# Optimization experiments

Measured on AMD Instinct MI355X. Metric: run time of the kernel, lower is better.

The kernel has to match this reference:

```python
import jax, jax.numpy as jnp
import numpy as np

H = 8          # num_heads
D = 64         # head_dim
HID = 512      # hidden_size
W = 128        # window_size
NEG = -1e9

def setup_inputs() -> dict:
    key = jax.random.key(0)
    ks = jax.random.split(key, 12)
    B, S = 2, 2048
    def lin(i):
        w = jax.random.normal(ks[i], (HID, HID), dtype=jnp.float32) * (1.0 / np.sqrt(HID))
        b = jax.random.normal(ks[i + 1], (HID,), dtype=jnp.float32) * 0.01
        return w, b
    Wq, bq = lin(0)
    Wk, bk = lin(2)
    Wv, bv = lin(4)
    Wo, bo = lin(6)
    return {
        "value": jax.random.normal(ks[8], (B, S, HID), dtype=jnp.float32),
        "key": jax.random.normal(ks[9], (B, S, HID), dtype=jnp.float32),
        "query": jax.random.normal(ks[10], (B, S, HID), dtype=jnp.float32),
        "Wq": Wq, "bq": bq, "Wk": Wk, "bk": bk,
        "Wv": Wv, "bv": bv, "Wo": Wo, "bo": bo,
    }

def reference(value, key, query, Wq, bq, Wk, bk, Wv, bv, Wo, bo):
    B, S, _ = query.shape
    def heads(x, Wt, b):
        # torch Linear: x @ W.T + b ; then [B,S,H,D] -> [B,H,S,D]
        return (x @ Wt.T + b).reshape(B, S, H, D).transpose(0, 2, 1, 3)
    Q = heads(query, Wq, bq)
    K = heads(key, Wk, bk)
    V = heads(value, Wv, bv)
    scores = jnp.einsum('bhqd,bhkd->bhqk', Q, K) / jnp.sqrt(jnp.float32(D))
    idx = jnp.arange(S)
    local = jnp.abs(idx[:, None] - idx[None, :]) <= W  # [S,S] band mask
    scores = jnp.where(local[None, None], scores, NEG)
    weights = jax.nn.softmax(scores, axis=-1)
    out = jnp.einsum('bhqk,bhkd->bhqd', weights, V)
    out = out.transpose(0, 2, 1, 3).reshape(B, S, HID)
    return out @ Wo.T + bo
```

## Files before the change

kernel.cpp:

```cpp
#include <hip/hip_runtime.h>
#include <stdint.h>

#define B_   2
#define S_   2048
#define H_   8
#define D_   64
#define HID_ 512
#define W_   128
#define M_   (B_ * S_)
#define E_   (M_ * HID_)
#define WSZ_ (HID_ * HID_)
#define PPAD_ 72
#define M0_  12.0f

typedef unsigned short u16;
typedef __attribute__((ext_vector_type(8))) __bf16 bf16x8;
typedef __attribute__((ext_vector_type(4))) float  floatx4;

__device__ __forceinline__ u16 f2b(float f) {
    union { __bf16 b; u16 u; } x;
    x.b = (__bf16)f;
    return x.u;
}

__device__ __forceinline__ void gll16(const u16* g, u16* l) {
    __builtin_amdgcn_global_load_lds(
        (const __attribute__((address_space(1))) unsigned int*)g,
        (__attribute__((address_space(3))) unsigned int*)l, 16, 0, 0);
}

__device__ __forceinline__ void cvt8_store(float4 a, float4 b, u16* dst) {
    bf16x8 v;
    v[0] = (__bf16)a.x; v[1] = (__bf16)a.y; v[2] = (__bf16)a.z; v[3] = (__bf16)a.w;
    v[4] = (__bf16)b.x; v[5] = (__bf16)b.y; v[6] = (__bf16)b.z; v[7] = (__bf16)b.w;
    *(bf16x8*)dst = v;
}

__global__ __launch_bounds__(256) void cvt_kernel(
    const float* __restrict__ q, const float* __restrict__ k, const float* __restrict__ v,
    const float* __restrict__ wq, const float* __restrict__ wk,
    const float* __restrict__ wv, const float* __restrict__ wo,
    u16* __restrict__ ws) {
    const int seg = blockIdx.y;
    const float* src; u16* dst; int n;
    switch (seg) {
        case 0:  src = q;  dst = ws + 4 * (size_t)E_;            n = E_;   break;
        case 1:  src = k;  dst = ws + 5 * (size_t)E_;            n = E_;   break;
        case 2:  src = v;  dst = ws + 6 * (size_t)E_;            n = E_;   break;
        case 3:  src = wq; dst = ws + 7 * (size_t)E_;            n = WSZ_; break;
        case 4:  src = wk; dst = ws + 7 * (size_t)E_ + WSZ_;     n = WSZ_; break;
        case 5:  src = wv; dst = ws + 7 * (size_t)E_ + 2 * WSZ_; n = WSZ_; break;
        default: src = wo; dst = ws + 7 * (size_t)E_ + 3 * WSZ_; n = WSZ_; break;
    }
    const int i = (blockIdx.x * 256 + threadIdx.x) * 8;
    if (i >= n) return;
    const float4* s = (const float4*)(src + i);
    cvt8_store(s[0], s[1], dst + i);
}

template <int MODE>
__device__ __forceinline__ void gemm_bf16_body(
    const u16* __restrict__ Ah, const u16* __restrict__ Bh,
    const float* __restrict__ bias, u16* __restrict__ outH,
    float* __restrict__ outF) {
    __shared__ u16 As[128 * 64];
    __shared__ u16 Bs[64 * 64];

    const int tid  = threadIdx.x;
    const int wave = tid >> 6;
    const int lane = tid & 63;
    const int r16  = lane & 15;
    const int quad = lane >> 4;
    const int m0 = blockIdx.x * 128;
    const int n0 = blockIdx.y * 64;
    const int m_base = m0 + wave * 64;

    floatx4 zero = {0.f, 0.f, 0.f, 0.f};
    floatx4 acc[4][4];
#pragma unroll
    for (int i = 0; i < 4; i++)
#pragma unroll
        for (int j = 0; j < 4; j++) acc[i][j] = zero;

    int aoff[2], boff[2];
#pragma unroll
    for (int ks = 0; ks < 2; ks++) {
        const int sw = (((ks * 4 + quad) ^ (r16 & 7)) * 8);
        aoff[ks] = (wave * 64 + r16) * 64 + sw;
        boff[ks] = r16 * 64 + sw;
    }

    for (int k0 = 0; k0 < HID_; k0 += 64) {
#pragma unroll
        for (int e = 0; e < 8; e++) {
            const int li = (wave * 8 + e) * 64 + lane;
            const int r  = li >> 3;
            const int cl = (li & 7) ^ (r & 7);
            gll16(Ah + (size_t)(m0 + r) * HID_ + k0 + cl * 8,
                  As + (size_t)(wave * 8 + e) * 512);
        }
#pragma unroll
        for (int e = 0; e < 4; e++) {
            const int li = (wave * 4 + e) * 64 + lane;
            const int r  = li >> 3;
            const int cl = (li & 7) ^ (r & 7);
            gll16(Bh + (size_t)(n0 + r) * HID_ + k0 + cl * 8,
                  Bs + (size_t)(wave * 4 + e) * 512);
        }
        __syncthreads();

        bf16x8 af[2][4], bf[2][4];
#pragma unroll
        for (int ks = 0; ks < 2; ks++)
#pragma unroll
            for (int t = 0; t < 4; t++) {
                af[ks][t] = *(const bf16x8*)&As[aoff[ks] + t * 1024];
                bf[ks][t] = *(const bf16x8*)&Bs[boff[ks] + t * 1024];
            }
#pragma unroll
        for (int ks = 0; ks < 2; ks++)
#pragma unroll
            for (int i = 0; i < 4; i++)
#pragma unroll
                for (int j = 0; j < 4; j++)
                    acc[i][j] = __builtin_amdgcn_mfma_f32_16x16x32_bf16(
                        af[ks][i], bf[ks][j], acc[i][j], 0, 0, 0);
        __syncthreads();
    }

    const int bb = m_base >> 11;
    if (MODE == 1) {
#pragma unroll
        for (int j = 0; j < 4; j++) {
            const int col = n0 + j * 16 + r16;
            const int h = col >> 6, d = col & (D_ - 1);
            const float bv = bias[col];
            const size_t base = (size_t)(bb * H_ + h) * S_;
#pragma unroll
            for (int i = 0; i < 4; i++)
#pragma unroll
                for (int r = 0; r < 4; r++) {
                    const int s = (m_base & (S_ - 1)) + i * 16 + quad * 4 + r;
                    outH[(base + s) * D_ + d] = f2b(acc[i][j][r] + bv);
                }
        }
    } else if (MODE == 2) {
#pragma unroll
        for (int j = 0; j < 4; j++) {
            const int col = n0 + j * 16 + r16;
            const int h = col >> 6, d = col & (D_ - 1);
            const float bv = bias[col];
            const size_t base = ((size_t)(bb * H_ + h) * D_ + d) * S_;
            const int s0 = (m_base & (S_ - 1)) + quad * 4;
#pragma unroll
            for (int i = 0; i < 4; i++) {
                ushort4 hs;
                hs.x = f2b(acc[i][j][0] + bv);
                hs.y = f2b(acc[i][j][1] + bv);
                hs.z = f2b(acc[i][j][2] + bv);
                hs.w = f2b(acc[i][j][3] + bv);
                *(ushort4*)(outH + base + s0 + i * 16) = hs;
            }
        }
    } else {
#pragma unroll
        for (int j = 0; j < 4; j++) {
            const int col = n0 + j * 16 + r16;
            const float bv = bias[col];
#pragma unroll
            for (int i = 0; i < 4; i++) {
                const int row0 = m_base + i * 16 + quad * 4;
#pragma unroll
                for (int r = 0; r < 4; r++)
                    outF[(size_t)(row0 + r) * HID_ + col] = acc[i][j][r] + bv;
            }
        }
    }
}

__global__ __launch_bounds__(128) void qkv_kernel(
    const u16* __restrict__ ws,
    const float* __restrict__ bq, const float* __restrict__ bk, const float* __restrict__ bv,
    u16* __restrict__ P) {
    const u16* X; const u16* Wt; const float* bias; u16* out;
    if (blockIdx.z == 0) {
        X = ws + 4 * (size_t)E_; Wt = ws + 7 * (size_t)E_;            bias = bq; out = P;
        gemm_bf16_body<1>(X, Wt, bias, out, nullptr);
    } else if (blockIdx.z == 1) {
        X = ws + 5 * (size_t)E_; Wt = ws + 7 * (size_t)E_ + WSZ_;     bias = bk; out = P + E_;
        gemm_bf16_body<1>(X, Wt, bias, out, nullptr);
    } else {
        X = ws + 6 * (size_t)E_; Wt = ws + 7 * (size_t)E_ + 2 * WSZ_; bias = bv; out = P + 2 * (size_t)E_;
        gemm_bf16_body<2>(X, Wt, bias, out, nullptr);
    }
}

__global__ __launch_bounds__(128) void out_kernel(
    const u16* __restrict__ AOh, const u16* __restrict__ Woh,
    const float* __restrict__ bias, float* __restrict__ outF) {
    gemm_bf16_body<3>(AOh, Woh, bias, nullptr, outF);
}

__global__ __launch_bounds__(256) void attn_kernel(
    const u16* __restrict__ Qh, const u16* __restrict__ Kh,
    const u16* __restrict__ Vth, u16* __restrict__ AOh) {
    __shared__ u16 Ps[4][16][PPAD_];
    __shared__ u16 Osh[4][16][PPAD_];

    const int tid  = threadIdx.x;
    const int wave = tid >> 6;
    const int lane = tid & 63;
    const int r16 = lane & 15, quad = lane >> 4;
    const int qt = blockIdx.x, bh = blockIdx.y;
    const int q0 = qt * 64 + wave * 16;
    const size_t sd = (size_t)bh * S_ * D_;
    const size_t ds = (size_t)bh * D_ * S_;

    bf16x8 qf[2];
#pragma unroll
    for (int ks = 0; ks < 2; ks++)
        qf[ks] = *(const bf16x8*)(Qh + sd + (size_t)(q0 + r16) * D_ + ks * 32 + quad * 8);

    floatx4 zero = {0.f, 0.f, 0.f, 0.f};
    floatx4 O[4];
    float lsum[4];
#pragma unroll
    for (int j = 0; j < 4; j++) O[j] = zero;
#pragma unroll
    for (int r = 0; r < 4; r++) lsum[r] = 0.f;

    int t_lo = qt - 2; if (t_lo < 0) t_lo = 0;
    int t_hi = qt + 2; if (t_hi > S_ / 64 - 1) t_hi = S_ / 64 - 1;

    for (int t = t_lo; t <= t_hi; ++t) {
        const int k0 = t * 64;
        floatx4 sa[4];
#pragma unroll
        for (int j = 0; j < 4; j++) sa[j] = zero;

#pragma unroll
        for (int ks = 0; ks < 2; ks++) {
            bf16x8 kf[4];
#pragma unroll
            for (int j = 0; j < 4; j++)
                kf[j] = *(const bf16x8*)(Kh + sd + (size_t)(k0 + j * 16 + r16) * D_ + ks * 32 + quad * 8);
#pragma unroll
            for (int j = 0; j < 4; j++)
                sa[j] = __builtin_amdgcn_mfma_f32_16x16x32_bf16(qf[ks], kf[j], sa[j], 0, 0, 0);
        }

#pragma unroll
        for (int j = 0; j < 4; j++) {
            const int kc = k0 + j * 16 + r16;
#pragma unroll
            for (int r = 0; r < 4; r++) {
                const int q = q0 + quad * 4 + r;
                const bool valid = (unsigned)(kc - q + W_) <= (unsigned)(2 * W_);
                const float p = valid ? __expf(fmaf(sa[j][r], 0.125f, -M0_)) : 0.f;
                lsum[r] += p;
                Ps[wave][quad * 4 + r][j * 16 + r16] = f2b(p);
            }
        }

#pragma unroll
        for (int ks = 0; ks < 2; ks++) {
            bf16x8 pf = *(const bf16x8*)&Ps[wave][r16][ks * 32 + quad * 8];
#pragma unroll
            for (int j = 0; j < 4; j++) {
                bf16x8 vf = *(const bf16x8*)(Vth + ds + (size_t)(j * 16 + r16) * S_ + k0 + ks * 32 + quad * 8);
                O[j] = __builtin_amdgcn_mfma_f32_16x16x32_bf16(pf, vf, O[j], 0, 0, 0);
            }
        }
    }

#pragma unroll
    for (int r = 0; r < 4; r++) {
        float l = lsum[r];
#pragma unroll
        for (int off = 1; off < 16; off <<= 1) l += __shfl_xor(l, off, 64);
        lsum[r] = l;
    }

#pragma unroll
    for (int r = 0; r < 4; r++) {
        const float linv = 1.f / lsum[r];
#pragma unroll
        for (int j = 0; j < 4; j++)
            Osh[wave][quad * 4 + r][j * 16 + r16] = f2b(O[j][r] * linv);
    }

    const int b = bh >> 3, h = bh & 7;
    const int qq = lane >> 2;
    const int d0 = (lane & 3) * 16;
    u16* dst = AOh + (size_t)(b * S_ + q0 + qq) * HID_ + h * D_ + d0;
    *(uint4*)dst       = *(const uint4*)&Osh[wave][qq][d0];
    *(uint4*)(dst + 8) = *(const uint4*)&Osh[wave][qq][d0 + 8];
}

extern "C" void kernel_launch(void* const* d_in, const int* in_sizes, int n_in,
                              void* d_out, int out_size, void* d_ws, size_t ws_size,
                              hipStream_t stream) {
    const float* value = (const float*)d_in[0];
    const float* key_  = (const float*)d_in[1];
    const float* query = (const float*)d_in[2];
    const float* Wq = (const float*)d_in[3];
    const float* bq = (const float*)d_in[4];
    const float* Wk = (const float*)d_in[5];
    const float* bk = (const float*)d_in[6];
    const float* Wv = (const float*)d_in[7];
    const float* bv = (const float*)d_in[8];
    const float* Wo = (const float*)d_in[9];
    const float* bo = (const float*)d_in[10];

    u16* ws  = (u16*)d_ws;
    u16* P   = ws;
    u16* AOh = ws + 3 * (size_t)E_;
    u16* Woh = ws + 7 * (size_t)E_ + 3 * (size_t)WSZ_;

    cvt_kernel<<<dim3(1024, 7), 256, 0, stream>>>(query, key_, value, Wq, Wk, Wv, Wo, ws);
    qkv_kernel<<<dim3(M_ / 128, HID_ / 64, 3), 128, 0, stream>>>(ws, bq, bk, bv, P);
    attn_kernel<<<dim3(S_ / 64, B_ * H_), 256, 0, stream>>>(
        P, P + E_, P + 2 * (size_t)E_, AOh);
    out_kernel<<<dim3(M_ / 128, HID_ / 64), 128, 0, stream>>>(AOh, Woh, bo, (float*)d_out);
}
```

Measured before the change: 139.2 us.

## Fuse conversion, QKV, attention and output GEMMs into one persistent kernel

Replaces the four launches (fp32→bf16 convert, QKV GEMM, attention, output GEMM) with a single 512-block kernel that separates phases with a software grid barrier built on an atomic counter. The GEMMs now read fp32 inputs and weights directly, converting them to bf16 in registers with a register-prefetch double buffer, so the separate conversion pass and its bf16 round trip through memory disappear. GEMM tiles grow to 128x128 with 4 waves, and the output GEMM uses only 128 blocks. The aim is to cut launch overhead and conversion traffic. The risks are idle blocks in the out phase, a barrier that assumes all 512 blocks are co-resident, and a bounded spin that could fall through silently.

Measured after the change: 237.9 us. 70.9% more time.

```diff
diff --git a/kernel.cpp b/kernel.cpp
--- a/kernel.cpp
+++ b/kernel.cpp
@@ -9,9 +9,10 @@
 #define W_   128
 #define M_   (B_ * S_)
 #define E_   (M_ * HID_)
-#define WSZ_ (HID_ * HID_)
 #define PPAD_ 72
 #define M0_  12.0f
+#define NBLK_ 512
+#define NTHR_ 256
 
 typedef unsigned short u16;
 typedef __attribute__((ext_vector_type(8))) __bf16 bf16x8;
@@ -36,44 +37,52 @@
     *(bf16x8*)dst = v;
 }
 
-__global__ __launch_bounds__(256) void cvt_kernel(
-    const float* __restrict__ q, const float* __restrict__ k, const float* __restrict__ v,
-    const float* __restrict__ wq, const float* __restrict__ wk,
-    const float* __restrict__ wv, const float* __restrict__ wo,
-    u16* __restrict__ ws) {
-    const int seg = blockIdx.y;
-    const float* src; u16* dst; int n;
-    switch (seg) {
-        case 0:  src = q;  dst = ws + 4 * (size_t)E_;            n = E_;   break;
-        case 1:  src = k;  dst = ws + 5 * (size_t)E_;            n = E_;   break;
-        case 2:  src = v;  dst = ws + 6 * (size_t)E_;            n = E_;   break;
-        case 3:  src = wq; dst = ws + 7 * (size_t)E_;            n = WSZ_; break;
-        case 4:  src = wk; dst = ws + 7 * (size_t)E_ + WSZ_;     n = WSZ_; break;
-        case 5:  src = wv; dst = ws + 7 * (size_t)E_ + 2 * WSZ_; n = WSZ_; break;
-        default: src = wo; dst = ws + 7 * (size_t)E_ + 3 * WSZ_; n = WSZ_; break;
-    }
-    const int i = (blockIdx.x * 256 + threadIdx.x) * 8;
-    if (i >= n) return;
-    const float4* s = (const float4*)(src + i);
-    cvt8_store(s[0], s[1], dst + i);
+__device__ __forceinline__ void gbar(unsigned* cnt, unsigned target) {
+    __syncthreads();
+    if (threadIdx.x == 0) {
+        __threadfence();
+        atomicAdd(cnt, 1u);
+        unsigned tries = 0;
+        while (atomicAdd(cnt, 0u) < target && ++tries < (1u << 22))
+            __builtin_amdgcn_s_sleep(2);
+        __threadfence();
+    }
+    __syncthreads();
+}
+
+__device__ __forceinline__ void frag_mfma(const u16* As, const u16* Bs,
+                                          const int aoff[2], const int boff[2],
+                                          floatx4 acc[4][4]) {
+    bf16x8 af[2][4], bf[2][4];
+#pragma unroll
+    for (int ks = 0; ks < 2; ks++)
+#pragma unroll
+        for (int t = 0; t < 4; t++) {
+            af[ks][t] = *(const bf16x8*)&As[aoff[ks] + t * 1024];
+            bf[ks][t] = *(const bf16x8*)&Bs[boff[ks] + t * 1024];
+        }
+#pragma unroll
+    for (int ks = 0; ks < 2; ks++)
+#pragma unroll
+        for (int i = 0; i < 4; i++)
+#pragma unroll
+            for (int j = 0; j < 4; j++)
+                acc[i][j] = __builtin_amdgcn_mfma_f32_16x16x32_bf16(
+                    af[ks][i], bf[ks][j], acc[i][j], 0, 0, 0);
 }
 
 template <int MODE>
-__device__ __forceinline__ void gemm_bf16_body(
-    const u16* __restrict__ Ah, const u16* __restrict__ Bh,
+__device__ __forceinline__ void gemm_qkv(
+    const float* __restrict__ Xf, const float* __restrict__ Wf,
     const float* __restrict__ bias, u16* __restrict__ outH,
-    float* __restrict__ outF) {
-    __shared__ u16 As[128 * 64];
-    __shared__ u16 Bs[64 * 64];
-
+    u16* As, u16* Bs, int m0, int n0) {
     const int tid  = threadIdx.x;
     const int wave = tid >> 6;
     const int lane = tid & 63;
     const int r16  = lane & 15;
     const int quad = lane >> 4;
-    const int m0 = blockIdx.x * 128;
-    const int n0 = blockIdx.y * 64;
-    const int m_base = m0 + wave * 64;
+    const int mq = (wave >> 1) * 64;
+    const int nq = (wave & 1) * 64;
 
     floatx4 zero = {0.f, 0.f, 0.f, 0.f};
     floatx4 acc[4][4];
@@ -86,53 +95,52 @@
 #pragma unroll
     for (int ks = 0; ks < 2; ks++) {
         const int sw = (((ks * 4 + quad) ^ (r16 & 7)) * 8);
-        aoff[ks] = (wave * 64 + r16) * 64 + sw;
-        boff[ks] = r16 * 64 + sw;
-    }
+        aoff[ks] = (mq + r16) * 64 + sw;
+        boff[ks] = (nq + r16) * 64 + sw;
+    }
+
+    const float* Xa = Xf + (size_t)m0 * HID_;
+    const float* Wb = Wf + (size_t)n0 * HID_;
+    float4 pa[8], pb[8];
+
+#define QLOAD(dst, Base, k0) do {                                              \
+        _Pragma("unroll")                                                      \
+        for (int e = 0; e < 4; e++) {                                          \
+            const int slot = e * 256 + tid;                                    \
+            const int r_ = slot >> 3, c_ = slot & 7;                           \
+            const float4* s_ = (const float4*)(Base + (size_t)r_ * HID_ + (k0) + c_ * 8); \
+            dst[2 * e] = s_[0]; dst[2 * e + 1] = s_[1];                        \
+        }                                                                      \
+    } while (0)
+
+    QLOAD(pa, Xa, 0);
+    QLOAD(pb, Wb, 0);
 
     for (int k0 = 0; k0 < HID_; k0 += 64) {
-#pragma unroll
-        for (int e = 0; e < 8; e++) {
-            const int li = (wave * 8 + e) * 64 + lane;
-            const int r  = li >> 3;
-            const int cl = (li & 7) ^ (r & 7);
-            gll16(Ah + (size_t)(m0 + r) * HID_ + k0 + cl * 8,
-                  As + (size_t)(wave * 8 + e) * 512);
-        }
+        __syncthreads();
 #pragma unroll
         for (int e = 0; e < 4; e++) {
-            const int li = (wave * 4 + e) * 64 + lane;
-            const int r  = li >> 3;
-            const int cl = (li & 7) ^ (r & 7);
-            gll16(Bh + (size_t)(n0 + r) * HID_ + k0 + cl * 8,
-                  Bs + (size_t)(wave * 4 + e) * 512);
+            const int slot = e * 256 + tid;
+            const int r_ = slot >> 3, c_ = slot & 7;
+            const int sw = r_ * 64 + ((c_ ^ (r_ & 7)) * 8);
+            cvt8_store(pa[2 * e], pa[2 * e + 1], &As[sw]);
+            cvt8_store(pb[2 * e], pb[2 * e + 1], &Bs[sw]);
         }
         __syncthreads();
-
-        bf16x8 af[2][4], bf[2][4];
-#pragma unroll
-        for (int ks = 0; ks < 2; ks++)
-#pragma unroll
-            for (int t = 0; t < 4; t++) {
-                af[ks][t] = *(const bf16x8*)&As[aoff[ks] + t * 1024];
-                bf[ks][t] = *(const bf16x8*)&Bs[boff[ks] + t * 1024];
-            }
-#pragma unroll
-        for (int ks = 0; ks < 2; ks++)
-#pragma unroll
-            for (int i = 0; i < 4; i++)
-#pragma unroll
-                for (int j = 0; j < 4; j++)
-                    acc[i][j] = __builtin_amdgcn_mfma_f32_16x16x32_bf16(
-                        af[ks][i], bf[ks][j], acc[i][j], 0, 0, 0);
-        __syncthreads();
-    }
-
+        if (k0 + 64 < HID_) {
+            QLOAD(pa, Xa, k0 + 64);
+            QLOAD(pb, Wb, k0 + 64);
+        }
+        frag_mfma(As, Bs, aoff, boff, acc);
+    }
+#undef QLOAD
+
+    const int m_base = m0 + mq;
     const int bb = m_base >> 11;
     if (MODE == 1) {
 #pragma unroll
         for (int j = 0; j < 4; j++) {
-            const int col = n0 + j * 16 + r16;
+            const int col = n0 + nq + j * 16 + r16;
             const int h = col >> 6, d = col & (D_ - 1);
             const float bv = bias[col];
             const size_t base = (size_t)(bb * H_ + h) * S_;
@@ -144,10 +152,10 @@
                     outH[(base + s) * D_ + d] = f2b(acc[i][j][r] + bv);
                 }
         }
-    } else if (MODE == 2) {
+    } else {
 #pragma unroll
         for (int j = 0; j < 4; j++) {
-            const int col = n0 + j * 16 + r16;
+            const int col = n0 + nq + j * 16 + r16;
             const int h = col >> 6, d = col & (D_ - 1);
             const float bv = bias[col];
             const size_t base = ((size_t)(bb * H_ + h) * D_ + d) * S_;
@@ -162,56 +170,91 @@
                 *(ushort4*)(outH + base + s0 + i * 16) = hs;
             }
         }
-    } else {
-#pragma unroll
-        for (int j = 0; j < 4; j++) {
-            const int col = n0 + j * 16 + r16;
-            const float bv = bias[col];
-#pragma unroll
-            for (int i = 0; i < 4; i++) {
-                const int row0 = m_base + i * 16 + quad * 4;
-#pragma unroll
-                for (int r = 0; r < 4; r++)
-                    outF[(size_t)(row0 + r) * HID_ + col] = acc[i][j][r] + bv;
-            }
-        }
-    }
-}
-
-__global__ __launch_bounds__(128) void qkv_kernel(
-    const u16* __restrict__ ws,
-    const float* __restrict__ bq, const float* __restrict__ bk, const float* __restrict__ bv,
-    u16* __restrict__ P) {
-    const u16* X; const u16* Wt; const float* bias; u16* out;
-    if (blockIdx.z == 0) {
-        X = ws + 4 * (size_t)E_; Wt = ws + 7 * (size_t)E_;            bias = bq; out = P;
-        gemm_bf16_body<1>(X, Wt, bias, out, nullptr);
-    } else if (blockIdx.z == 1) {
-        X = ws + 5 * (size_t)E_; Wt = ws + 7 * (size_t)E_ + WSZ_;     bias = bk; out = P + E_;
-        gemm_bf16_body<1>(X, Wt, bias, out, nullptr);
-    } else {
-        X = ws + 6 * (size_t)E_; Wt = ws + 7 * (size_t)E_ + 2 * WSZ_; bias = bv; out = P + 2 * (size_t)E_;
-        gemm_bf16_body<2>(X, Wt, bias, out, nullptr);
-    }
-}
-
-__global__ __launch_bounds__(128) void out_kernel(
-    const u16* __restrict__ AOh, const u16* __restrict__ Woh,
-    const float* __restrict__ bias, float* __restrict__ outF) {
-    gemm_bf16_body<3>(AOh, Woh, bias, nullptr, outF);
-}
-
-__global__ __launch_bounds__(256) void attn_kernel(
-    const u16* __restrict__ Qh, const u16* __restrict__ Kh,
-    const u16* __restrict__ Vth, u16* __restrict__ AOh) {
-    __shared__ u16 Ps[4][16][PPAD_];
-    __shared__ u16 Osh[4][16][PPAD_];
-
+    }
+}
+
+__device__ __forceinline__ void gemm_out(
+    const u16* __restrict__ AOh, const float* __restrict__ Wf,
+    const float* __restrict__ bias, float* __restrict__ outF,
+    u16* As, u16* Bs, int m0, int n0) {
     const int tid  = threadIdx.x;
     const int wave = tid >> 6;
     const int lane = tid & 63;
-    const int r16 = lane & 15, quad = lane >> 4;
-    const int qt = blockIdx.x, bh = blockIdx.y;
+    const int r16  = lane & 15;
+    const int quad = lane >> 4;
+    const int mq = (wave >> 1) * 64;
+    const int nq = (wave & 1) * 64;
+
+    floatx4 zero = {0.f, 0.f, 0.f, 0.f};
+    floatx4 acc[4][4];
+#pragma unroll
+    for (int i = 0; i < 4; i++)
+#pragma unroll
+        for (int j = 0; j < 4; j++) acc[i][j] = zero;
+
+    int aoff[2], boff[2];
+#pragma unroll
+    for (int ks = 0; ks < 2; ks++) {
+        const int sw = (((ks * 4 + quad) ^ (r16 & 7)) * 8);
+        aoff[ks] = (mq + r16) * 64 + sw;
+        boff[ks] = (nq + r16) * 64 + sw;
+    }
+
+    const float* Wb = Wf + (size_t)n0 * HID_;
+    float4 pb[8];
+#define OLOADB(k0) do {                                                        \
+        _Pragma("unroll")                                                      \
+        for (int e = 0; e < 4; e++) {                                          \
+            const int slot = e * 256 + tid;                                    \
+            const int r_ = slot >> 3, c_ = slot & 7;                           \
+            const float4* s_ = (const float4*)(Wb + (size_t)r_ * HID_ + (k0) + c_ * 8); \
+            pb[2 * e] = s_[0]; pb[2 * e + 1] = s_[1];                          \
+        }                                                                      \
+    } while (0)
+
+    OLOADB(0);
+    for (int k0 = 0; k0 < HID_; k0 += 64) {
+        __syncthreads();
+#pragma unroll
+        for (int e = 0; e < 4; e++) {
+            const int li = (wave * 4 + e) * 64 + lane;
+            const int r_ = li >> 3;
+            const int cl = (li & 7) ^ (r_ & 7);
+            gll16(AOh + (size_t)(m0 + r_) * HID_ + k0 + cl * 8,
+                  As + (size_t)(wave * 4 + e) * 512);
+        }
+#pragma unroll
+        for (int e = 0; e < 4; e++) {
+            const int slot = e * 256 + tid;
+            const int r_ = slot >> 3, c_ = slot & 7;
+            cvt8_store(pb[2 * e], pb[2 * e + 1], &Bs[r_ * 64 + ((c_ ^ (r_ & 7)) * 8)]);
+        }
+        __syncthreads();
+        if (k0 + 64 < HID_) OLOADB(k0 + 64);
+        frag_mfma(As, Bs, aoff, boff, acc);
+    }
+#undef OLOADB
+
+    const int m_base = m0 + mq;
+#pragma unroll
+    for (int j = 0; j < 4; j++) {
+        const int col = n0 + nq + j * 16 + r16;
+        const float bv = bias[col];
+#pragma unroll
+        for (int i = 0; i < 4; i++) {
+            const int row0 = m_base + i * 16 + quad * 4;
+#pragma unroll
+            for (int r = 0; r < 4; r++)
+                outF[(size_t)(row0 + r) * HID_ + col] = acc[i][j][r] + bv;
+        }
+    }
+}
+
+__device__ __forceinline__ void attn_unit(
+    int u, const u16* __restrict__ Qh, const u16* __restrict__ Kh,
+    const u16* __restrict__ Vth, u16* __restrict__ AOh,
+    u16* Psw, u16* Oshw, int wave, int lane, int r16, int quad) {
+    const int qt = u & 31, bh = u >> 5;
     const int q0 = qt * 64 + wave * 16;
     const size_t sd = (size_t)bh * S_ * D_;
     const size_t ds = (size_t)bh * D_ * S_;
@@ -258,13 +301,13 @@
                 const bool valid = (unsigned)(kc - q + W_) <= (unsigned)(2 * W_);
                 const float p = valid ? __expf(fmaf(sa[j][r], 0.125f, -M0_)) : 0.f;
                 lsum[r] += p;
-                Ps[wave][quad * 4 + r][j * 16 + r16] = f2b(p);
+                Psw[(quad * 4 + r) * PPAD_ + j * 16 + r16] = f2b(p);
             }
         }
 
 #pragma unroll
         for (int ks = 0; ks < 2; ks++) {
-            bf16x8 pf = *(const bf16x8*)&Ps[wave][r16][ks * 32 + quad * 8];
+            bf16x8 pf = *(const bf16x8*)&Psw[r16 * PPAD_ + ks * 32 + quad * 8];
 #pragma unroll
             for (int j = 0; j < 4; j++) {
                 bf16x8 vf = *(const bf16x8*)(Vth + ds + (size_t)(j * 16 + r16) * S_ + k0 + ks * 32 + quad * 8);
@@ -286,15 +329,57 @@
         const float linv = 1.f / lsum[r];
 #pragma unroll
         for (int j = 0; j < 4; j++)
-            Osh[wave][quad * 4 + r][j * 16 + r16] = f2b(O[j][r] * linv);
+            Oshw[(quad * 4 + r) * PPAD_ + j * 16 + r16] = f2b(O[j][r] * linv);
     }
 
     const int b = bh >> 3, h = bh & 7;
     const int qq = lane >> 2;
     const int d0 = (lane & 3) * 16;
     u16* dst = AOh + (size_t)(b * S_ + q0 + qq) * HID_ + h * D_ + d0;
-    *(uint4*)dst       = *(const uint4*)&Osh[wave][qq][d0];
-    *(uint4*)(dst + 8) = *(const uint4*)&Osh[wave][qq][d0 + 8];
+    *(uint4*)dst       = *(const uint4*)&Oshw[qq * PPAD_ + d0];
+    *(uint4*)(dst + 8) = *(const uint4*)&Oshw[qq * PPAD_ + d0 + 8];
+}
+
+__global__ __launch_bounds__(NTHR_, 2) void fused_kernel(
+    const float* __restrict__ xq, const float* __restrict__ xk, const float* __restrict__ xv,
+    const float* __restrict__ wq, const float* __restrict__ wk,
+    const float* __restrict__ wv, const float* __restrict__ wo,
+    const float* __restrict__ bq, const float* __restrict__ bk,
+    const float* __restrict__ bvv, const float* __restrict__ bo,
+    u16* __restrict__ ws, float* __restrict__ outF, unsigned* __restrict__ bar) {
+
+    __shared__ union {
+        struct { u16 As[128 * 64]; u16 Bs[128 * 64]; } g;
+        struct { u16 Ps[4][16][PPAD_]; u16 Osh[4][16][PPAD_]; } a;
+    } sm;
+
+    const int bid  = blockIdx.x;
+    const int tid  = threadIdx.x;
+    const int wave = tid >> 6;
+    const int lane = tid & 63;
+    const int r16 = lane & 15, quad = lane >> 4;
+
+    if (bid < 384) {
+        const int z = bid >> 7, rem = bid & 127;
+        const int m0 = (rem & 31) * 128, n0 = (rem >> 5) * 128;
+        const float* Xf = z == 0 ? xq : z == 1 ? xk : xv;
+        const float* Wf = z == 0 ? wq : z == 1 ? wk : wv;
+        const float* bias = z == 0 ? bq : z == 1 ? bk : bvv;
+        u16* out = ws + (size_t)z * E_;
+        if (z < 2) gemm_qkv<1>(Xf, Wf, bias, out, sm.g.As, sm.g.Bs, m0, n0);
+        else       gemm_qkv<2>(Xf, Wf, bias, out, sm.g.As, sm.g.Bs, m0, n0);
+    }
+    gbar(bar, NBLK_);
+
+    for (int u = bid; u < 512; u += NBLK_)
+        attn_unit(u, ws, ws + (size_t)E_, ws + 2 * (size_t)E_, ws + 3 * (size_t)E_,
+                  &sm.a.Ps[wave][0][0], &sm.a.Osh[wave][0][0], wave, lane, r16, quad);
+    gbar(bar, 2u * NBLK_);
+
+    if (bid < 128) {
+        const int m0 = (bid & 31) * 128, n0 = (bid >> 5) * 128;
+        gemm_out(ws + 3 * (size_t)E_, wo, bo, outF, sm.g.As, sm.g.Bs, m0, n0);
+    }
 }
 
 extern "C" void kernel_launch(void* const* d_in, const int* in_sizes, int n_in,
@@ -312,14 +397,11 @@
     const float* Wo = (const float*)d_in[9];
     const float* bo = (const float*)d_in[10];
 
-    u16* ws  = (u16*)d_ws;
-    u16* P   = ws;
-    u16* AOh = ws + 3 * (size_t)E_;
-    u16* Woh = ws + 7 * (size_t)E_ + 3 * (size_t)WSZ_;
-
-    cvt_kernel<<<dim3(1024, 7), 256, 0, stream>>>(query, key_, value, Wq, Wk, Wv, Wo, ws);
-    qkv_kernel<<<dim3(M_ / 128, HID_ / 64, 3), 128, 0, stream>>>(ws, bq, bk, bv, P);
-    attn_kernel<<<dim3(S_ / 64, B_ * H_), 256, 0, stream>>>(
-        P, P + E_, P + 2 * (size_t)E_, AOh);
-    out_kernel<<<dim3(M_ / 128, HID_ / 64), 128, 0, stream>>>(AOh, Woh, bo, (float*)d_out);
-}
+    u16* ws = (u16*)d_ws;
+    unsigned* bar = (unsigned*)(ws + 4 * (size_t)E_);
+
+    hipMemsetAsync((void*)bar, 0, 256, stream);
+    fused_kernel<<<dim3(NBLK_), dim3(NTHR_), 0, stream>>>(
+        query, key_, value, Wq, Wk, Wv, Wo, bq, bk, bv, bo,
+        ws, (float*)d_out, bar);
+}
```
